# Kernel tuning notes

Measured on AMD Instinct MI355X. Metric: run time of the kernel, lower is better.

The kernel has to match this reference:

```python
import jax, jax.numpy as jnp
import numpy as np

X_SIZE = 256
H_SIZE = 512
N_CHILDREN = 32768


def setup_inputs() -> dict:
    key = jax.random.key(0)
    ks = jax.random.split(key, 7)
    x = jax.random.normal(ks[0], (X_SIZE,), dtype=jnp.float32)
    hs = jax.random.normal(ks[1], (N_CHILDREN, H_SIZE), dtype=jnp.float32)
    cs = jax.random.normal(ks[2], (N_CHILDREN, H_SIZE), dtype=jnp.float32)
    # xavier-uniform-ish init for weights, zeros for biases
    def xavier(k, shape):
        fan_in, fan_out = shape[-1], shape[-2]
        limit = float(np.sqrt(6.0 / (fan_in + fan_out)))
        return jax.random.uniform(k, shape, jnp.float32, -limit, limit)
    w_iou = xavier(ks[3], (3, H_SIZE, X_SIZE))
    u_iou = xavier(ks[4], (3, H_SIZE, H_SIZE))
    b_iou = jnp.zeros((3, H_SIZE), jnp.float32)
    w_f = xavier(ks[5], (H_SIZE, X_SIZE))
    u_f = xavier(ks[6], (H_SIZE, H_SIZE))
    b_f = jnp.zeros((H_SIZE, 1), jnp.float32)
    return {"x": x, "hs": hs, "cs": cs, "w_iou": w_iou, "u_iou": u_iou,
            "b_iou": b_iou, "w_f": w_f, "u_f": u_f, "b_f": b_f}


def reference(x, hs, cs, w_iou, u_iou, b_iou, w_f, u_f, b_f):
    # Child-sum Tree-LSTM cell for a single node.
    h_sum = hs.sum(axis=0)                                    # (h,)
    iou = (jnp.einsum('khx,x->kh', w_iou, x)
           + jnp.einsum('khg,g->kh', u_iou, h_sum)
           + b_iou)                                            # (3, h)
    i, o, u = iou[0], iou[1], iou[2]
    # fs: (h, n_children) forget gates, one per child
    fs = (w_f @ x)[:, None] + jnp.einsum('hg,ng->hn', u_f, hs) + b_f
    i = jax.nn.sigmoid(i)
    o = jax.nn.sigmoid(o)
    fs = jax.nn.sigmoid(fs)
    u = jnp.tanh(u)
    c = i * u + jnp.sum(fs * cs.T, axis=1)                    # (h,)
    h = o * jnp.tanh(c)
    return (h, c)
```

## Files before the change

### kernel.cpp

```cpp
#include <hip/hip_runtime.h>
#include <stdint.h>
#include <stddef.h>

#define H 512
#define XD 256
#define NCHLD 32768
#define NB 64
#define NSHARD 32

#define WS_PREF 0
#define WS_IOU  512
#define WS_CACC 2048
#define WS_HSUM 18432
#define WS_UF16 34816

typedef float f32x4 __attribute__((ext_vector_type(4)));
typedef _Float16 f16x8 __attribute__((ext_vector_type(8)));
typedef _Float16 f16x4 __attribute__((ext_vector_type(4)));

__device__ __forceinline__ float sigm(float x) { return 1.0f / (1.0f + __expf(-x)); }

__global__ __launch_bounds__(256) void k0_setup(const float* __restrict__ x,
                                                const float* __restrict__ w_f,
                                                const float* __restrict__ b_f,
                                                const float* __restrict__ u_f,
                                                float* __restrict__ ws) {
    const int b = blockIdx.x;
    if (b < 256) {
        const int i = (b * 256 + threadIdx.x) * 4;
        float4 v = *(const float4*)(u_f + i);
        f16x4 h;
        h[0] = (_Float16)v.x; h[1] = (_Float16)v.y;
        h[2] = (_Float16)v.z; h[3] = (_Float16)v.w;
        *(f16x4*)((_Float16*)(ws + WS_UF16) + i) = h;
    } else {
        const int gid = (b - 256) * 256 + threadIdx.x;
        const int row = gid >> 2;
        const int part = gid & 3;
        const float4* wr = (const float4*)(w_f + (size_t)row * XD) + part * 16;
        const float4* xv = (const float4*)x + part * 16;
        float acc = 0.0f;
#pragma unroll 4
        for (int i = 0; i < 16; ++i) {
            float4 a = wr[i], c = xv[i];
            acc += a.x * c.x + a.y * c.y + a.z * c.z + a.w * c.w;
        }
        acc += __shfl_xor(acc, 1);
        acc += __shfl_xor(acc, 2);
        if (part == 0) ws[WS_PREF + row] = acc + b_f[row];
        float4 z = make_float4(0.f, 0.f, 0.f, 0.f);
#pragma unroll
        for (int t = 0; t < 4; ++t)
            ((float4*)ws)[512 + gid * 4 + t] = z;
    }
}

__global__ __launch_bounds__(512, 2) void k2_main(const float* __restrict__ hs,
                                                  const float* __restrict__ cs,
                                                  float* __restrict__ ws) {
    __shared__ _Float16 Bs[NB * H];
    __shared__ float hsum_l[H];

    const _Float16* uf16 = (const _Float16*)(ws + WS_UF16);
    const float* pre_f = ws + WS_PREF;
    float* c_acc   = ws + WS_CACC + (blockIdx.x & (NSHARD - 1)) * H;
    float* h_shard = ws + WS_HSUM + (blockIdx.x & (NSHARD - 1)) * H;

    const int tid  = threadIdx.x;
    const int wid  = tid >> 6;
    const int lane = tid & 63;
    const int c0   = blockIdx.x * NB;
    const int fc   = lane & 15;
    const int q    = lane >> 4;

    hsum_l[tid] = 0.0f;
    __syncthreads();

    {
        const float4* g0 = (const float4*)hs + (((size_t)(c0 + wid)) << 7) + (lane << 1);
        _Float16* w0 = Bs + (wid << 9) + ((lane ^ wid) << 3);
        float4 r[16];
#pragma unroll
        for (int j = 0; j < 8; ++j) {
            r[2 * j]     = g0[(size_t)j << 10];
            r[2 * j + 1] = g0[((size_t)j << 10) + 1];
        }
        float4 ha = make_float4(0.f, 0.f, 0.f, 0.f);
        float4 hb = make_float4(0.f, 0.f, 0.f, 0.f);
#pragma unroll
        for (int j = 0; j < 8; ++j) {
            float4 lo = r[2 * j], hi = r[2 * j + 1];
            f16x8 hv;
            hv[0] = (_Float16)lo.x; hv[1] = (_Float16)lo.y;
            hv[2] = (_Float16)lo.z; hv[3] = (_Float16)lo.w;
            hv[4] = (_Float16)hi.x; hv[5] = (_Float16)hi.y;
            hv[6] = (_Float16)hi.z; hv[7] = (_Float16)hi.w;
            *(f16x8*)(w0 + (j << 12)) = hv;
            ha.x += lo.x; ha.y += lo.y; ha.z += lo.z; ha.w += lo.w;
            hb.x += hi.x; hb.y += hi.y; hb.z += hi.z; hb.w += hi.w;
        }
        float* hd = &hsum_l[lane * 8];
        atomicAdd(hd + 0, ha.x); atomicAdd(hd + 1, ha.y);
        atomicAdd(hd + 2, ha.z); atomicAdd(hd + 3, ha.w);
        atomicAdd(hd + 4, hb.x); atomicAdd(hd + 5, hb.y);
        atomicAdd(hd + 6, hb.z); atomicAdd(hd + 7, hb.w);
    }
    __syncthreads();

    atomicAdd(&h_shard[tid], hsum_l[tid]);

    float4 csr[4][4];
#pragma unroll
    for (int rt = 0; rt < 4; ++rt)
#pragma unroll
        for (int ct = 0; ct < 4; ++ct) {
            const int child = c0 + ct * 16 + fc;
            const int rglob = wid * 64 + rt * 16 + q * 4;
            csr[rt][ct] = *(const float4*)(cs + (size_t)child * H + rglob);
        }

    f32x4 acc[4][4];
    const f32x4 vzero = {0.0f, 0.0f, 0.0f, 0.0f};
#pragma unroll
    for (int rt = 0; rt < 4; ++rt)
#pragma unroll
        for (int ct = 0; ct < 4; ++ct)
            acc[rt][ct] = vzero;

    const _Float16* abase = uf16 + (size_t)(wid * 64 + fc) * H + q * 8;

#pragma unroll
    for (int kk = 0; kk < 16; ++kk) {
        f16x8 af[4];
#pragma unroll
        for (int rt = 0; rt < 4; ++rt)
            af[rt] = *(const f16x8*)(abase + (size_t)rt * 16 * H + kk * 32);
        f16x8 bf[4];
#pragma unroll
        for (int ct = 0; ct < 4; ++ct) {
            const int ch = ct * 16 + fc;
            bf[ct] = *(const f16x8*)(Bs + ch * H + (((kk * 4 + q) ^ (fc & 7)) << 3));
        }
#pragma unroll
        for (int ct = 0; ct < 4; ++ct)
#pragma unroll
            for (int rt = 0; rt < 4; ++rt)
                acc[rt][ct] = __builtin_amdgcn_mfma_f32_16x16x32_f16(af[rt], bf[ct], acc[rt][ct], 0, 0, 0);
    }

#pragma unroll
    for (int rt = 0; rt < 4; ++rt) {
        const int rglob = wid * 64 + rt * 16 + q * 4;
        float4 pf = *(const float4*)(pre_f + rglob);
        f32x4 csum = vzero;
#pragma unroll
        for (int ct = 0; ct < 4; ++ct) {
            float4 cv = csr[rt][ct];
            csum[0] += sigm(acc[rt][ct][0] + pf.x) * cv.x;
            csum[1] += sigm(acc[rt][ct][1] + pf.y) * cv.y;
            csum[2] += sigm(acc[rt][ct][2] + pf.z) * cv.z;
            csum[3] += sigm(acc[rt][ct][3] + pf.w) * cv.w;
        }
#pragma unroll
        for (int m = 1; m <= 8; m <<= 1) {
            csum[0] += __shfl_xor(csum[0], m); csum[1] += __shfl_xor(csum[1], m);
            csum[2] += __shfl_xor(csum[2], m); csum[3] += __shfl_xor(csum[3], m);
        }
        if (fc == 0) {
            atomicAdd(&c_acc[rglob + 0], csum[0]); atomicAdd(&c_acc[rglob + 1], csum[1]);
            atomicAdd(&c_acc[rglob + 2], csum[2]); atomicAdd(&c_acc[rglob + 3], csum[3]);
        }
    }
}

__global__ __launch_bounds__(256) void k3_iou(const float* __restrict__ x,
                                              const float* __restrict__ w_iou,
                                              const float* __restrict__ u_iou,
                                              const float* __restrict__ b_iou,
                                              float* __restrict__ ws) {
    __shared__ float h_red[H];
    const int tid = threadIdx.x;
    {
        float a0 = 0.0f, a1 = 0.0f;
#pragma unroll 8
        for (int s = 0; s < NSHARD; ++s) {
            a0 += ws[WS_HSUM + s * H + tid * 2 + 0];
            a1 += ws[WS_HSUM + s * H + tid * 2 + 1];
        }
        h_red[tid * 2 + 0] = a0;
        h_red[tid * 2 + 1] = a1;
    }
    __syncthreads();

    const int gid = blockIdx.x * 256 + tid;
    const int row = gid >> 4;
    const int part = gid & 15;
    float acc = 0.0f;
    const float4* wr = (const float4*)(w_iou + (size_t)row * XD) + part * 4;
    const float4* xv = (const float4*)x + part * 4;
#pragma unroll
    for (int i = 0; i < 4; ++i) {
        float4 a = wr[i], b = xv[i];
        acc += a.x * b.x + a.y * b.y + a.z * b.z + a.w * b.w;
    }
    const float4* ur = (const float4*)(u_iou + (size_t)row * H) + part * 8;
    const float4* hv = (const float4*)h_red + part * 8;
#pragma unroll
    for (int i = 0; i < 8; ++i) {
        float4 a = ur[i], b = hv[i];
        acc += a.x * b.x + a.y * b.y + a.z * b.z + a.w * b.w;
    }
    acc += __shfl_xor(acc, 1);
    acc += __shfl_xor(acc, 2);
    acc += __shfl_xor(acc, 4);
    acc += __shfl_xor(acc, 8);
    if (part == 0) ws[WS_IOU + row] = acc + b_iou[row];
}

__global__ __launch_bounds__(512) void k4_fin(const float* __restrict__ ws,
                                              float* __restrict__ out) {
    const int h = threadIdx.x;
    float cacc = 0.0f;
#pragma unroll 8
    for (int s = 0; s < NSHARD; ++s) cacc += ws[WS_CACC + s * H + h];
    const float i = sigm(ws[WS_IOU + h]);
    const float o = sigm(ws[WS_IOU + 512 + h]);
    const float u = tanhf(ws[WS_IOU + 1024 + h]);
    const float c = i * u + cacc;
    out[h]       = o * tanhf(c);
    out[512 + h] = c;
}

extern "C" void kernel_launch(void* const* d_in, const int* in_sizes, int n_in,
                              void* d_out, int out_size, void* d_ws, size_t ws_size,
                              hipStream_t stream) {
    const float* x     = (const float*)d_in[0];
    const float* hs    = (const float*)d_in[1];
    const float* cs    = (const float*)d_in[2];
    const float* w_iou = (const float*)d_in[3];
    const float* u_iou = (const float*)d_in[4];
    const float* b_iou = (const float*)d_in[5];
    const float* w_f   = (const float*)d_in[6];
    const float* u_f   = (const float*)d_in[7];
    const float* b_f   = (const float*)d_in[8];
    float* ws  = (float*)d_ws;
    float* out = (float*)d_out;

    k0_setup<<<264, 256, 0, stream>>>(x, w_f, b_f, u_f, ws);
    k2_main<<<NCHLD / NB, 512, 0, stream>>>(hs, cs, ws);
    k3_iou<<<96, 256, 0, stream>>>(x, w_iou, u_iou, b_iou, ws);
    k4_fin<<<1, 512, 0, stream>>>(ws, out);
}
```

Baseline: 215.4 us.

## Split forget-gate GEMM rows across two smaller blocks with 32 children each

```diff
diff --git a/kernel.cpp b/kernel.cpp
--- a/kernel.cpp
+++ b/kernel.cpp
@@ -5,7 +5,8 @@
 #define H 512
 #define XD 256
 #define NCHLD 32768
-#define NB 64
+#define NB 32
+#define MROWS 256
 #define NSHARD 32
 
 #define WS_PREF 0
@@ -16,7 +17,6 @@
 
 typedef float f32x4 __attribute__((ext_vector_type(4)));
 typedef _Float16 f16x8 __attribute__((ext_vector_type(8)));
-typedef _Float16 f16x4 __attribute__((ext_vector_type(4)));
 
 __device__ __forceinline__ float sigm(float x) { return 1.0f / (1.0f + __expf(-x)); }
 
@@ -29,10 +29,10 @@
     if (b < 256) {
         const int i = (b * 256 + threadIdx.x) * 4;
         float4 v = *(const float4*)(u_f + i);
-        f16x4 h;
-        h[0] = (_Float16)v.x; h[1] = (_Float16)v.y;
-        h[2] = (_Float16)v.z; h[3] = (_Float16)v.w;
-        *(f16x4*)((_Float16*)(ws + WS_UF16) + i) = h;
+        _Float16 h0 = (_Float16)v.x, h1 = (_Float16)v.y;
+        _Float16 h2 = (_Float16)v.z, h3 = (_Float16)v.w;
+        _Float16* dst = (_Float16*)(ws + WS_UF16) + i;
+        dst[0] = h0; dst[1] = h1; dst[2] = h2; dst[3] = h3;
     } else {
         const int gid = (b - 256) * 256 + threadIdx.x;
         const int row = gid >> 2;
@@ -55,7 +55,7 @@
     }
 }
 
-__global__ __launch_bounds__(512, 2) void k2_main(const float* __restrict__ hs,
+__global__ __launch_bounds__(256, 4) void k2_main(const float* __restrict__ hs,
                                                   const float* __restrict__ cs,
                                                   float* __restrict__ ws) {
     __shared__ _Float16 Bs[NB * H];
@@ -63,71 +63,75 @@
 
     const _Float16* uf16 = (const _Float16*)(ws + WS_UF16);
     const float* pre_f = ws + WS_PREF;
-    float* c_acc   = ws + WS_CACC + (blockIdx.x & (NSHARD - 1)) * H;
-    float* h_shard = ws + WS_HSUM + (blockIdx.x & (NSHARD - 1)) * H;
+    const int bid   = blockIdx.x;
+    const int ntile = bid >> 1;
+    const int mtile = bid & 1;
+    const int c0    = ntile * NB;
+    const int r0    = mtile * MROWS;
+    float* c_acc = ws + WS_CACC + (bid & (NSHARD - 1)) * H;
 
     const int tid  = threadIdx.x;
     const int wid  = tid >> 6;
     const int lane = tid & 63;
-    const int c0   = blockIdx.x * NB;
     const int fc   = lane & 15;
     const int q    = lane >> 4;
 
     hsum_l[tid] = 0.0f;
+    hsum_l[tid + 256] = 0.0f;
     __syncthreads();
 
     {
-        const float4* g0 = (const float4*)hs + (((size_t)(c0 + wid)) << 7) + (lane << 1);
-        _Float16* w0 = Bs + (wid << 9) + ((lane ^ wid) << 3);
-        float4 r[16];
-#pragma unroll
-        for (int j = 0; j < 8; ++j) {
-            r[2 * j]     = g0[(size_t)j << 10];
-            r[2 * j + 1] = g0[((size_t)j << 10) + 1];
-        }
+        const float* g0 = hs + (size_t)(c0 + wid * 8) * H + lane * 8;
+        _Float16* wbase = Bs + (size_t)(wid * 8) * H + ((lane ^ 0) * 0);
         float4 ha = make_float4(0.f, 0.f, 0.f, 0.f);
         float4 hb = make_float4(0.f, 0.f, 0.f, 0.f);
 #pragma unroll
-        for (int j = 0; j < 8; ++j) {
-            float4 lo = r[2 * j], hi = r[2 * j + 1];
-            f16x8 hv;
-            hv[0] = (_Float16)lo.x; hv[1] = (_Float16)lo.y;
-            hv[2] = (_Float16)lo.z; hv[3] = (_Float16)lo.w;
-            hv[4] = (_Float16)hi.x; hv[5] = (_Float16)hi.y;
-            hv[6] = (_Float16)hi.z; hv[7] = (_Float16)hi.w;
-            *(f16x8*)(w0 + (j << 12)) = hv;
-            ha.x += lo.x; ha.y += lo.y; ha.z += lo.z; ha.w += lo.w;
-            hb.x += hi.x; hb.y += hi.y; hb.z += hi.z; hb.w += hi.w;
-        }
-        float* hd = &hsum_l[lane * 8];
-        atomicAdd(hd + 0, ha.x); atomicAdd(hd + 1, ha.y);
-        atomicAdd(hd + 2, ha.z); atomicAdd(hd + 3, ha.w);
-        atomicAdd(hd + 4, hb.x); atomicAdd(hd + 5, hb.y);
-        atomicAdd(hd + 6, hb.z); atomicAdd(hd + 7, hb.w);
+        for (int half = 0; half < 2; ++half) {
+            float4 ra[4], rb[4];
+#pragma unroll
+            for (int j = 0; j < 4; ++j) {
+                const int cj = half * 4 + j;
+                ra[j] = *(const float4*)(g0 + (size_t)cj * H);
+                rb[j] = *(const float4*)(g0 + (size_t)cj * H + 4);
+            }
+#pragma unroll
+            for (int j = 0; j < 4; ++j) {
+                const int cj = half * 4 + j;
+                f16x8 hv;
+                hv[0] = (_Float16)ra[j].x; hv[1] = (_Float16)ra[j].y;
+                hv[2] = (_Float16)ra[j].z; hv[3] = (_Float16)ra[j].w;
+                hv[4] = (_Float16)rb[j].x; hv[5] = (_Float16)rb[j].y;
+                hv[6] = (_Float16)rb[j].z; hv[7] = (_Float16)rb[j].w;
+                *(f16x8*)(Bs + (size_t)(wid * 8 + cj) * H + ((lane ^ cj) << 3)) = hv;
+                ha.x += ra[j].x; ha.y += ra[j].y; ha.z += ra[j].z; ha.w += ra[j].w;
+                hb.x += rb[j].x; hb.y += rb[j].y; hb.z += rb[j].z; hb.w += rb[j].w;
+            }
+        }
+        if (mtile == 0) {
+            float* hd = &hsum_l[lane * 8];
+            atomicAdd(hd + 0, ha.x); atomicAdd(hd + 1, ha.y);
+            atomicAdd(hd + 2, ha.z); atomicAdd(hd + 3, ha.w);
+            atomicAdd(hd + 4, hb.x); atomicAdd(hd + 5, hb.y);
+            atomicAdd(hd + 6, hb.z); atomicAdd(hd + 7, hb.w);
+        }
     }
     __syncthreads();
 
-    atomicAdd(&h_shard[tid], hsum_l[tid]);
-
-    float4 csr[4][4];
-#pragma unroll
-    for (int rt = 0; rt < 4; ++rt)
-#pragma unroll
-        for (int ct = 0; ct < 4; ++ct) {
-            const int child = c0 + ct * 16 + fc;
-            const int rglob = wid * 64 + rt * 16 + q * 4;
-            csr[rt][ct] = *(const float4*)(cs + (size_t)child * H + rglob);
-        }
-
-    f32x4 acc[4][4];
+    if (mtile == 0) {
+        float* shard = ws + WS_HSUM + (ntile & (NSHARD - 1)) * H;
+        atomicAdd(&shard[tid], hsum_l[tid]);
+        atomicAdd(&shard[tid + 256], hsum_l[tid + 256]);
+    }
+
+    f32x4 acc[4][2];
     const f32x4 vzero = {0.0f, 0.0f, 0.0f, 0.0f};
 #pragma unroll
-    for (int rt = 0; rt < 4; ++rt)
-#pragma unroll
-        for (int ct = 0; ct < 4; ++ct)
-            acc[rt][ct] = vzero;
-
-    const _Float16* abase = uf16 + (size_t)(wid * 64 + fc) * H + q * 8;
+    for (int rt = 0; rt < 4; ++rt) {
+        acc[rt][0] = vzero;
+        acc[rt][1] = vzero;
+    }
+
+    const _Float16* abase = uf16 + (size_t)(r0 + wid * 64 + fc) * H + q * 8;
 
 #pragma unroll
     for (int kk = 0; kk < 16; ++kk) {
@@ -135,14 +139,12 @@
 #pragma unroll
         for (int rt = 0; rt < 4; ++rt)
             af[rt] = *(const f16x8*)(abase + (size_t)rt * 16 * H + kk * 32);
-        f16x8 bf[4];
-#pragma unroll
-        for (int ct = 0; ct < 4; ++ct) {
-            const int ch = ct * 16 + fc;
-            bf[ct] = *(const f16x8*)(Bs + ch * H + (((kk * 4 + q) ^ (fc & 7)) << 3));
-        }
-#pragma unroll
-        for (int ct = 0; ct < 4; ++ct)
+        f16x8 bf[2];
+#pragma unroll
+        for (int ct = 0; ct < 2; ++ct)
+            bf[ct] = *(const f16x8*)(Bs + (size_t)(ct * 16 + fc) * H + (((kk * 4 + q) ^ (fc & 7)) << 3));
+#pragma unroll
+        for (int ct = 0; ct < 2; ++ct)
 #pragma unroll
             for (int rt = 0; rt < 4; ++rt)
                 acc[rt][ct] = __builtin_amdgcn_mfma_f32_16x16x32_f16(af[rt], bf[ct], acc[rt][ct], 0, 0, 0);
@@ -150,12 +152,13 @@
 
 #pragma unroll
     for (int rt = 0; rt < 4; ++rt) {
-        const int rglob = wid * 64 + rt * 16 + q * 4;
+        const int rglob = r0 + wid * 64 + rt * 16 + q * 4;
         float4 pf = *(const float4*)(pre_f + rglob);
         f32x4 csum = vzero;
 #pragma unroll
-        for (int ct = 0; ct < 4; ++ct) {
-            float4 cv = csr[rt][ct];
+        for (int ct = 0; ct < 2; ++ct) {
+            const int child = c0 + ct * 16 + fc;
+            float4 cv = *(const float4*)(cs + (size_t)child * H + rglob);
             csum[0] += sigm(acc[rt][ct][0] + pf.x) * cv.x;
             csum[1] += sigm(acc[rt][ct][1] + pf.y) * cv.y;
             csum[2] += sigm(acc[rt][ct][2] + pf.z) * cv.z;
@@ -247,7 +250,7 @@
     float* out = (float*)d_out;
 
     k0_setup<<<264, 256, 0, stream>>>(x, w_f, b_f, u_f, ws);
-    k2_main<<<NCHLD / NB, 512, 0, stream>>>(hs, cs, ws);
+    k2_main<<<(NCHLD / NB) * 2, 256, 0, stream>>>(hs, cs, ws);
     k3_iou<<<96, 256, 0, stream>>>(x, w_iou, u_iou, b_iou, ws);
     k4_fin<<<1, 512, 0, stream>>>(ws, out);
 }
```

New measurement: 243.5 us. 13.1% more time.
